# Optimization experiments

Measured on AMD Instinct MI355X. Metric: run time of the kernel, lower is better.

Reference implementation:

```python
import jax, jax.numpy as jnp
import numpy as np

B, S, H, W, T, D = 256, 128, 14, 14, 12, 512


def _lin(key, fan_in, fan_out):
    k1, k2 = jax.random.split(key)
    bound = 1.0 / np.sqrt(fan_in)
    Wm = jax.random.uniform(k1, (fan_in, fan_out), jnp.float32, -bound, bound)
    b = jax.random.uniform(k2, (fan_out,), jnp.float32, -bound, bound)
    return Wm, b


def setup_inputs() -> dict:
    key = jax.random.key(0)
    ks = jax.random.split(key, 20)
    inp = {
        "ci_1": jax.random.normal(ks[0], (B, D), jnp.float32),
        "mi_1": jax.random.normal(ks[1], (B, D), jnp.float32),
        "q": jax.random.normal(ks[2], (B, D), jnp.float32),
        "cws": jax.random.normal(ks[3], (B, S, D), jnp.float32),
        "K": jax.random.normal(ks[4], (B, H, W, D), jnp.float32),
        "C_past": jax.random.normal(ks[5], (B, T, D), jnp.float32),
        "M_past": jax.random.normal(ks[6], (B, T, D), jnp.float32),
    }
    inp["W_cq"], inp["b_cq"] = _lin(ks[7], D, D)          # control_qi
    inp["W_cqi"], inp["b_cqi"] = _lin(ks[8], 2 * D, D)    # cqi_linear
    inp["W_cai"], inp["b_cai"] = _lin(ks[9], D, 1)        # cais_linear
    inp["W_rm"], inp["b_rm"] = _lin(ks[10], D, D)         # memory_read_m
    inp["W_rk"], inp["b_rk"] = _lin(ks[11], D, D)         # memory_read_k
    inp["W_rik"], inp["b_rik"] = _lin(ks[12], 2 * D, D)   # memory_read_ik
    inp["W_rci"], inp["b_rci"] = _lin(ks[13], D, D)       # memory_read_ci_i
    inp["W_wrm"], inp["b_wrm"] = _lin(ks[14], 2 * D, D)   # memory_write_ri_mi_1
    inp["W_wcc"], inp["b_wcc"] = _lin(ks[15], D, 1)       # memory_write_ci_cj
    inp["W_wsa"], inp["b_wsa"] = _lin(ks[16], D, D)       # memory_write_mi_sa
    inp["W_winfo"], inp["b_winfo"] = _lin(ks[17], D, D)   # memory_write_mi_info
    inp["W_wci"], inp["b_wci"] = _lin(ks[18], D, 1)       # memory_write_ci
    return inp


def reference(ci_1, mi_1, q, cws, K, C_past, M_past,
              W_cq, b_cq, W_cqi, b_cqi, W_cai, b_cai,
              W_rm, b_rm, W_rk, b_rk, W_rik, b_rik, W_rci, b_rci,
              W_wrm, b_wrm, W_wcc, b_wcc, W_wsa, b_wsa,
              W_winfo, b_winfo, W_wci, b_wci):
    # ---- control ----
    qi = q @ W_cq + b_cq                                        # [B,D]
    cqi = jnp.concatenate([ci_1, qi], axis=1) @ W_cqi + b_cqi   # [B,D]
    cqi_cws = cqi[:, None, :] * cws                             # [B,S,D]
    cai = cqi_cws @ W_cai + b_cai                               # [B,S,1]
    cvis = jax.nn.softmax(cai, axis=1)
    ci = (cvis * cws).sum(axis=1)                               # [B,D]

    # ---- read ----
    Ii = (mi_1 @ W_rm + b_rm)[:, None, None, :] * (K @ W_rk + b_rk)  # [B,H,W,D]
    Ii_prime = jnp.concatenate([Ii, K], axis=3) @ W_rik + b_rik      # [B,H,W,D]
    rai = (ci[:, None, None, :] * Ii_prime) @ W_rci + b_rci          # [B,H,W,D]
    rvi = jax.nn.softmax(rai, axis=1)   # softmax over H
    rvi = jax.nn.softmax(rvi, axis=2)   # then softmax of those probs over W (faithful)
    ri = (rvi * K).sum(axis=(1, 2))                                  # [B,D]

    # ---- write ----
    mi_info = jnp.concatenate([ri, mi_1], axis=1) @ W_wrm + b_wrm    # [B,D]
    ci_cj = ci[:, None, :] * C_past                                  # [B,T,D]
    saij = jax.nn.softmax(ci_cj @ W_wcc + b_wcc, axis=1)             # [B,T,1]
    mi_sa = (saij * M_past).sum(axis=1)                              # [B,D]
    mi_prime = (mi_sa @ W_wsa + b_wsa) + (mi_info @ W_winfo + b_winfo)
    gate = jax.nn.sigmoid(ci @ W_wci + b_wci)                        # [B,1]
    mi = gate * mi_1 + (1.0 - gate) * mi_prime
    return (ci, mi)
```

## Files before the change

kernel.cpp:

```cpp
#include <hip/hip_runtime.h>
#include <hip/hip_bf16.h>

typedef unsigned short u16;
typedef __attribute__((ext_vector_type(8))) short short8;
typedef __attribute__((ext_vector_type(4))) float f4;

static __device__ __forceinline__ float b2f(u16 u) {
    union { unsigned int i; float f; } x; x.i = ((unsigned int)u) << 16; return x.f;
}
static __device__ __forceinline__ u16 f2b(float f) {
    union { float f; unsigned int i; } x; x.f = f;
    unsigned int r = x.i + 0x7fffu + ((x.i >> 16) & 1u);
    return (u16)(r >> 16);
}
static __device__ __forceinline__ float wave_reduce_sum(float v) {
    #pragma unroll
    for (int off = 32; off > 0; off >>= 1) v += __shfl_down(v, off, 64);
    return v;
}
static __device__ __forceinline__ void gl2lds(const void* g, void* l) {
    __builtin_amdgcn_global_load_lds(
        (const __attribute__((address_space(1))) void*)g,
        (__attribute__((address_space(3))) void*)l, 16, 0, 0);
}

__global__ __launch_bounds__(256) void conv_f32_bf16(
    const float* __restrict__ src, u16* __restrict__ dst, int n)
{
    int i = (blockIdx.x * 256 + threadIdx.x) * 4;
    if (i >= n) return;
    float4 v = *(const float4*)(src + i);
    union { u16 u[4]; uint2 d; } o;
    o.u[0] = f2b(v.x); o.u[1] = f2b(v.y); o.u[2] = f2b(v.z); o.u[3] = f2b(v.w);
    *(uint2*)(dst + i) = o.d;
}

__global__ __launch_bounds__(256) void transpose_k(
    const float* __restrict__ in, u16* __restrict__ out,
    int K, int N, int out_stride, int k_off)
{
    __shared__ float t[32][33];
    int kb = blockIdx.x * 32, nb = blockIdx.y * 32;
    int tx = threadIdx.x, ty = threadIdx.y;
    #pragma unroll
    for (int i = 0; i < 4; i++)
        t[ty + i * 8][tx] = in[(size_t)(kb + ty + i * 8) * N + nb + tx];
    __syncthreads();
    #pragma unroll
    for (int i = 0; i < 4; i++)
        out[(size_t)(nb + ty + i * 8) * out_stride + k_off + kb + tx] =
            f2b(t[tx][ty + i * 8]);
}

template<int MT, int NT>
__global__ __launch_bounds__(256) void gemm_mfma(
    const u16* __restrict__ A0, const u16* __restrict__ A1,
    int M, int K0, int K1, int N,
    const u16* __restrict__ Bt,
    const float* __restrict__ bias0, const float* __restrict__ bias1,
    int epi_mode, const float* __restrict__ E, int m_div,
    const float* __restrict__ gate, const float* __restrict__ mi1,
    void* __restrict__ Cout, int out_f32)
{
    constexpr int BM = MT * 32, BN = NT * 32;
    constexpr int STG = (BM + BN) * 32;
    constexpr int NPF = MT / 2 + NT / 2;
    constexpr int STAGE_B = 3 * STG * 2;
    constexpr int EP_B = (MT == 4) ? 32 * 260 * 4 : 0;
    __shared__ __align__(16) char smem[(STAGE_B > EP_B) ? STAGE_B : EP_B];
    short* stg = (short*)smem;
    float* ep  = (float*)smem;

    int tid  = threadIdx.x;
    int wave = tid >> 6, lane = tid & 63;
    int wm = wave >> 1, wn = wave & 1;
    int lrow = lane & 15, quad = lane >> 4;

    int gx = gridDim.x, gy = gridDim.y;
    int bx = blockIdx.x, by = blockIdx.y;
    if ((gy & 7) == 0) {
        int lin = by * gx + bx;
        int xcd = lin & 7, j = lin >> 3;
        by = xcd * (gy >> 3) + j / gx;
        bx = j % gx;
    }
    int bm0 = by * BM, bn0 = bx * BN;
    int Ktot = K0 + K1;
    int KT = Ktot >> 5;

    int r16 = lane >> 2, cc = lane & 3;
    int sw = (r16 >> 1) & 3;
    int coff = (cc ^ sw) * 8;

    auto stage = [&](int s, int k0) {
        const u16* asrc; int lda;
        if (k0 < K0) { asrc = A0 + k0; lda = K0; }
        else         { asrc = A1 + (k0 - K0); lda = K1; }
        short* As = stg + s * STG;
        short* Bs = As + BM * 32;
        #pragma unroll
        for (int i = 0; i < MT / 2; i++) {
            int ar = wave * (BM / 4) + 16 * i;
            gl2lds(asrc + (size_t)(bm0 + ar + r16) * lda + coff, As + ar * 32);
        }
        #pragma unroll
        for (int i = 0; i < NT / 2; i++) {
            int br = wave * (BN / 4) + 16 * i;
            gl2lds(Bt + (size_t)(bn0 + br + r16) * Ktot + k0 + coff, Bs + br * 32);
        }
    };

    f4 acc[MT][NT];
    #pragma unroll
    for (int i = 0; i < MT; i++)
        #pragma unroll
        for (int j = 0; j < NT; j++)
            acc[i][j] = (f4){0.f, 0.f, 0.f, 0.f};

    stage(0, 0);
    if (KT > 1) stage(1, 32);
    int sb = 0;
    int sw2 = (lrow >> 1) & 3;
    for (int kt = 0; kt < KT; kt++) {
        if (kt + 1 < KT) {
            if constexpr (NPF == 6)
                asm volatile("s_waitcnt vmcnt(6) lgkmcnt(0)\ns_barrier" ::: "memory");
            else if constexpr (NPF == 4)
                asm volatile("s_waitcnt vmcnt(4) lgkmcnt(0)\ns_barrier" ::: "memory");
            else if constexpr (NPF == 2)
                asm volatile("s_waitcnt vmcnt(2) lgkmcnt(0)\ns_barrier" ::: "memory");
            else
                asm volatile("s_waitcnt vmcnt(0) lgkmcnt(0)\ns_barrier" ::: "memory");
        } else {
            asm volatile("s_waitcnt vmcnt(0) lgkmcnt(0)\ns_barrier" ::: "memory");
        }
        const short* Ab = stg + sb * STG;
        const short* Bb = Ab + BM * 32;
        if (kt + 2 < KT) {
            int s2 = sb + 2; if (s2 >= 3) s2 -= 3;
            stage(s2, (kt + 2) * 32);
        }
        short8 af[MT], bfr[NT];
        #pragma unroll
        for (int mt = 0; mt < MT; mt++)
            af[mt] = *(const short8*)&Ab[(wm * (MT * 16) + mt * 16 + lrow) * 32 + (quad ^ sw2) * 8];
        #pragma unroll
        for (int nt = 0; nt < NT; nt++)
            bfr[nt] = *(const short8*)&Bb[(wn * (NT * 16) + nt * 16 + lrow) * 32 + (quad ^ sw2) * 8];
        #pragma unroll
        for (int mt = 0; mt < MT; mt++)
            #pragma unroll
            for (int nt = 0; nt < NT; nt++)
                acc[mt][nt] = __builtin_amdgcn_mfma_f32_16x16x32_bf16(
                    af[mt], bfr[nt], acc[mt][nt], 0, 0, 0);
        sb = (sb + 1 == 3) ? 0 : sb + 1;
    }

    if constexpr (MT == 4) {
        __syncthreads();
        int rr = tid >> 3, c8 = tid & 7;
        #pragma unroll
        for (int p = 0; p < 4; p++) {
            if (wm == (p >> 1)) {
                #pragma unroll
                for (int mh = 0; mh < 2; mh++) {
                    int mt = 2 * (p & 1) + mh;
                    int lm = mh * 16 + quad * 4;
                    #pragma unroll
                    for (int nt = 0; nt < NT; nt++) {
                        int col = wn * (NT * 16) + nt * 16 + lrow;
                        #pragma unroll
                        for (int r = 0; r < 4; r++)
                            ep[(lm + r) * 260 + col] = acc[mt][nt][r];
                    }
                }
            }
            __syncthreads();
            int m = bm0 + p * 32 + rr;
            #pragma unroll
            for (int i = 0; i < NT; i++) {
                int ci = i * 8 + c8;
                int n = bn0 + ci * 4;
                float4 v = *(const float4*)&ep[rr * 260 + ci * 4];
                if (bias0) {
                    float4 bb = *(const float4*)&bias0[n];
                    v.x += bb.x; v.y += bb.y; v.z += bb.z; v.w += bb.w;
                }
                if (bias1) {
                    float4 bb = *(const float4*)&bias1[n];
                    v.x += bb.x; v.y += bb.y; v.z += bb.z; v.w += bb.w;
                }
                if (epi_mode == 1) {
                    float4 e = *(const float4*)(E + (size_t)(m / m_div) * N + n);
                    v.x *= e.x; v.y *= e.y; v.z *= e.z; v.w *= e.w;
                } else if (epi_mode == 2) {
                    float g = gate[m];
                    float4 mm = *(const float4*)(mi1 + (size_t)m * N + n);
                    v.x = g * mm.x + (1.f - g) * v.x;
                    v.y = g * mm.y + (1.f - g) * v.y;
                    v.z = g * mm.z + (1.f - g) * v.z;
                    v.w = g * mm.w + (1.f - g) * v.w;
                }
                if (out_f32) {
                    *(float4*)((float*)Cout + (size_t)m * N + n) = v;
                } else {
                    union { u16 u[4]; uint2 d; } o;
                    o.u[0] = f2b(v.x); o.u[1] = f2b(v.y);
                    o.u[2] = f2b(v.z); o.u[3] = f2b(v.w);
                    *(uint2*)((u16*)Cout + (size_t)m * N + n) = o.d;
                }
            }
            __syncthreads();
        }
    } else {
        #pragma unroll
        for (int nt = 0; nt < NT; nt++) {
            int n = bn0 + wn * (NT * 16) + nt * 16 + lrow;
            float bv = 0.f;
            if (bias0) bv += bias0[n];
            if (bias1) bv += bias1[n];
            #pragma unroll
            for (int mt = 0; mt < MT; mt++) {
                #pragma unroll
                for (int r = 0; r < 4; r++) {
                    int m = bm0 + wm * (MT * 16) + mt * 16 + quad * 4 + r;
                    float v = acc[mt][nt][r] + bv;
                    if (epi_mode == 1) {
                        v *= E[(size_t)(m / m_div) * N + n];
                    } else if (epi_mode == 2) {
                        float g = gate[m];
                        v = g * mi1[(size_t)m * N + n] + (1.f - g) * v;
                    }
                    if (out_f32) ((float*)Cout)[(size_t)m * N + n] = v;
                    else         ((u16*)Cout)[(size_t)m * N + n] = f2b(v);
                }
            }
        }
    }
}

__global__ __launch_bounds__(256) void control_attn(
    const float* __restrict__ cqi, const float* __restrict__ cws,
    const float* __restrict__ Wcai, const float* __restrict__ bcai,
    float* __restrict__ ci_f32, float* __restrict__ ci_out)
{
    int b = blockIdx.x, tid = threadIdx.x;
    __shared__ float tW[512];
    __shared__ float p[128];
    __shared__ float inv_l;
    for (int d = tid; d < 512; d += 256)
        tW[d] = cqi[(size_t)b * 512 + d] * Wcai[d];
    __syncthreads();
    int wave = tid >> 6, lane = tid & 63;
    const float* cwsb = cws + (size_t)b * 128 * 512;
    for (int s = wave; s < 128; s += 4) {
        const float* row = cwsb + (size_t)s * 512 + lane * 8;
        float acc = 0.f;
        #pragma unroll
        for (int j = 0; j < 8; j++) acc += tW[lane * 8 + j] * row[j];
        acc = wave_reduce_sum(acc);
        if (lane == 0) p[s] = acc + bcai[0];
    }
    __syncthreads();
    if (tid == 0) {
        float m = -1e30f;
        for (int s = 0; s < 128; s++) m = fmaxf(m, p[s]);
        float l = 0.f;
        for (int s = 0; s < 128; s++) { float e = __expf(p[s] - m); p[s] = e; l += e; }
        inv_l = 1.f / l;
    }
    __syncthreads();
    float inv = inv_l;
    for (int d = tid; d < 512; d += 256) {
        float acc = 0.f;
        for (int s = 0; s < 128; s++) acc += p[s] * cwsb[(size_t)s * 512 + d];
        acc *= inv;
        ci_f32[(size_t)b * 512 + d] = acc;
        ci_out[(size_t)b * 512 + d] = acc;
    }
}

__global__ __launch_bounds__(256) void read_reduce(
    const u16* __restrict__ rai, const u16* __restrict__ Kb, u16* __restrict__ ri)
{
    int b = blockIdx.x >> 1;
    int d = ((blockIdx.x & 1) << 8) + threadIdx.x;
    const u16* rb = rai + (size_t)b * 196 * 512 + d;
    const u16* kb = Kb + (size_t)b * 196 * 512 + d;
    float m1[14], il1[14];
    #pragma unroll
    for (int w = 0; w < 14; w++) {
        float m = -1e30f, s = 0.f;
        #pragma unroll
        for (int h = 0; h < 14; h++) {
            float v = b2f(rb[(size_t)(h * 14 + w) * 512]);
            float nm = fmaxf(m, v);
            s = s * __expf(m - nm) + __expf(v - nm);
            m = nm;
        }
        m1[w] = m; il1[w] = 1.f / s;
    }
    float acc = 0.f;
    #pragma unroll
    for (int h = 0; h < 14; h++) {
        float pv[14], ss = 0.f;
        #pragma unroll
        for (int w = 0; w < 14; w++) {
            float pr = __expf(b2f(rb[(size_t)(h * 14 + w) * 512]) - m1[w]) * il1[w];
            float e = __expf(pr);
            pv[w] = e; ss += e;
        }
        float il2 = 1.f / ss;
        #pragma unroll
        for (int w = 0; w < 14; w++)
            acc += pv[w] * il2 * b2f(kb[(size_t)(h * 14 + w) * 512]);
    }
    ri[(size_t)b * 512 + d] = f2b(acc);
}

__global__ __launch_bounds__(256) void write_attn(
    const float* __restrict__ ci_f32, const float* __restrict__ C_past,
    const float* __restrict__ M_past,
    const float* __restrict__ Wwcc, const float* __restrict__ bwcc,
    const float* __restrict__ Wwci, const float* __restrict__ bwci,
    u16* __restrict__ mi_sa, float* __restrict__ gate)
{
    int b = blockIdx.x, tid = threadIdx.x;
    __shared__ float c[512];
    __shared__ float pt[12];
    __shared__ float red[256];
    for (int d = tid; d < 512; d += 256) c[d] = ci_f32[(size_t)b * 512 + d];
    __syncthreads();
    float g = 0.f;
    for (int d = tid; d < 512; d += 256) g += c[d] * Wwci[d];
    red[tid] = g;
    __syncthreads();
    for (int s = 128; s > 0; s >>= 1) {
        if (tid < s) red[tid] += red[tid + s];
        __syncthreads();
    }
    int wave = tid >> 6, lane = tid & 63;
    const float* cp = C_past + (size_t)b * 12 * 512;
    for (int t = wave; t < 12; t += 4) {
        float acc = 0.f;
        #pragma unroll
        for (int j = 0; j < 8; j++) {
            int d = lane * 8 + j;
            acc += c[d] * Wwcc[d] * cp[(size_t)t * 512 + d];
        }
        acc = wave_reduce_sum(acc);
        if (lane == 0) pt[t] = acc + bwcc[0];
    }
    __syncthreads();
    if (tid == 0) {
        float m = -1e30f;
        for (int t = 0; t < 12; t++) m = fmaxf(m, pt[t]);
        float l = 0.f;
        for (int t = 0; t < 12; t++) { float e = __expf(pt[t] - m); pt[t] = e; l += e; }
        float invl = 1.f / l;
        for (int t = 0; t < 12; t++) pt[t] *= invl;
        gate[b] = 1.f / (1.f + __expf(-(red[0] + bwci[0])));
    }
    __syncthreads();
    const float* mp = M_past + (size_t)b * 12 * 512;
    for (int d = tid; d < 512; d += 256) {
        float acc = 0.f;
        #pragma unroll
        for (int t = 0; t < 12; t++) acc += pt[t] * mp[(size_t)t * 512 + d];
        mi_sa[(size_t)b * 512 + d] = f2b(acc);
    }
}

extern "C" void kernel_launch(void* const* d_in, const int* in_sizes, int n_in,
                              void* d_out, int out_size, void* d_ws, size_t ws_size,
                              hipStream_t stream) {
    (void)in_sizes; (void)n_in; (void)out_size;
    const int B = 256, D = 512, HW = 196;

    const float* ci_1   = (const float*)d_in[0];
    const float* mi_1   = (const float*)d_in[1];
    const float* q      = (const float*)d_in[2];
    const float* cws    = (const float*)d_in[3];
    const float* Kin    = (const float*)d_in[4];
    const float* C_past = (const float*)d_in[5];
    const float* M_past = (const float*)d_in[6];
    const float* W_cq   = (const float*)d_in[7];
    const float* b_cq   = (const float*)d_in[8];
    const float* W_cqi  = (const float*)d_in[9];
    const float* b_cqi  = (const float*)d_in[10];
    const float* W_cai  = (const float*)d_in[11];
    const float* b_cai  = (const float*)d_in[12];
    const float* W_rm   = (const float*)d_in[13];
    const float* b_rm   = (const float*)d_in[14];
    const float* W_rk   = (const float*)d_in[15];
    const float* b_rk   = (const float*)d_in[16];
    const float* W_rik  = (const float*)d_in[17];
    const float* b_rik  = (const float*)d_in[18];
    const float* W_rci  = (const float*)d_in[19];
    const float* b_rci  = (const float*)d_in[20];
    const float* W_wrm  = (const float*)d_in[21];
    const float* b_wrm  = (const float*)d_in[22];
    const float* W_wcc  = (const float*)d_in[23];
    const float* b_wcc  = (const float*)d_in[24];
    const float* W_wsa  = (const float*)d_in[25];
    const float* b_wsa  = (const float*)d_in[26];
    const float* W_winfo= (const float*)d_in[27];
    const float* b_winfo= (const float*)d_in[28];
    const float* W_wci  = (const float*)d_in[29];
    const float* b_wci  = (const float*)d_in[30];

    float* out_ci = (float*)d_out;
    float* out_mi = (float*)d_out + (size_t)B * D;

    char* ws = (char*)d_ws;
    size_t off = 0;
    auto alloc = [&](size_t bytes) -> void* {
        void* p = ws + off; off += (bytes + 255) & ~(size_t)255; return p;
    };
    u16* wt_cq    = (u16*)alloc((size_t)D * D * 2);
    u16* wt_cqi   = (u16*)alloc((size_t)D * 2 * D * 2);
    u16* wt_rm    = (u16*)alloc((size_t)D * D * 2);
    u16* wt_rk    = (u16*)alloc((size_t)D * D * 2);
    u16* wt_rik   = (u16*)alloc((size_t)D * 2 * D * 2);
    u16* wt_rci   = (u16*)alloc((size_t)D * D * 2);
    u16* wt_wrm   = (u16*)alloc((size_t)D * 2 * D * 2);
    u16* wt_wsi   = (u16*)alloc((size_t)D * 2 * D * 2);
    u16* qb       = (u16*)alloc((size_t)B * D * 2);
    u16* cib      = (u16*)alloc((size_t)B * D * 2);
    u16* mib      = (u16*)alloc((size_t)B * D * 2);
    u16* qi_buf   = (u16*)alloc((size_t)B * D * 2);
    float* cqi_f32= (float*)alloc((size_t)B * D * 4);
    float* rm_f32 = (float*)alloc((size_t)B * D * 4);
    float* ci_f32 = (float*)alloc((size_t)B * D * 4);
    u16* ri_buf   = (u16*)alloc((size_t)B * D * 2);
    u16* misa_buf = (u16*)alloc((size_t)B * D * 2);
    u16* minfo_buf= (u16*)alloc((size_t)B * D * 2);
    float* gate_b = (float*)alloc((size_t)B * 4);

    int chunk_b = 256;
    while (chunk_b > 32) {
        size_t need = off + 3 * (((size_t)chunk_b * HW * D * 2 + 255) & ~(size_t)255);
        if (need <= ws_size) break;
        chunk_b >>= 1;
    }
    u16* kbf  = (u16*)alloc((size_t)chunk_b * HW * D * 2);
    u16* big1 = (u16*)alloc((size_t)chunk_b * HW * D * 2);
    u16* big2 = (u16*)alloc((size_t)chunk_b * HW * D * 2);

    dim3 tb(32, 8);
    transpose_k<<<dim3(D / 32, D / 32), tb, 0, stream>>>(W_cq,   wt_cq,  D,     D, D,     0);
    transpose_k<<<dim3(2 * D / 32, D / 32), tb, 0, stream>>>(W_cqi, wt_cqi, 2 * D, D, 2 * D, 0);
    transpose_k<<<dim3(D / 32, D / 32), tb, 0, stream>>>(W_rm,   wt_rm,  D,     D, D,     0);
    transpose_k<<<dim3(D / 32, D / 32), tb, 0, stream>>>(W_rk,   wt_rk,  D,     D, D,     0);
    transpose_k<<<dim3(2 * D / 32, D / 32), tb, 0, stream>>>(W_rik, wt_rik, 2 * D, D, 2 * D, 0);
    transpose_k<<<dim3(D / 32, D / 32), tb, 0, stream>>>(W_rci,  wt_rci, D,     D, D,     0);
    transpose_k<<<dim3(2 * D / 32, D / 32), tb, 0, stream>>>(W_wrm, wt_wrm, 2 * D, D, 2 * D, 0);
    transpose_k<<<dim3(D / 32, D / 32), tb, 0, stream>>>(W_wsa,  wt_wsi, D,     D, 2 * D, 0);
    transpose_k<<<dim3(D / 32, D / 32), tb, 0, stream>>>(W_winfo,wt_wsi, D,     D, 2 * D, D);

    int nbd = B * D;
    conv_f32_bf16<<<nbd / 1024, 256, 0, stream>>>(q, qb, nbd);
    conv_f32_bf16<<<nbd / 1024, 256, 0, stream>>>(ci_1, cib, nbd);
    conv_f32_bf16<<<nbd / 1024, 256, 0, stream>>>(mi_1, mib, nbd);

    dim3 gsmall(D / 64, B / 64);

    gemm_mfma<2,2><<<gsmall, 256, 0, stream>>>(qb, nullptr, B, D, 0, D, wt_cq, b_cq, nullptr,
                                               0, nullptr, 1, nullptr, nullptr, qi_buf, 0);
    gemm_mfma<2,2><<<gsmall, 256, 0, stream>>>(cib, qi_buf, B, D, D, D, wt_cqi, b_cqi, nullptr,
                                               0, nullptr, 1, nullptr, nullptr, cqi_f32, 1);
    control_attn<<<B, 256, 0, stream>>>(cqi_f32, cws, W_cai, b_cai, ci_f32, out_ci);
    gemm_mfma<2,2><<<gsmall, 256, 0, stream>>>(mib, nullptr, B, D, 0, D, wt_rm, b_rm, nullptr,
                                               0, nullptr, 1, nullptr, nullptr, rm_f32, 1);

    for (int c = 0; c < B; c += chunk_b) {
        int mrows = chunk_b * HW;
        const float* Kc = Kin + (size_t)c * HW * D;
        conv_f32_bf16<<<(mrows * D) / 1024, 256, 0, stream>>>(Kc, kbf, mrows * D);
        dim3 gbig(D / 128, mrows / 128);
        gemm_mfma<4,4><<<gbig, 256, 0, stream>>>(kbf, nullptr, mrows, D, 0, D, wt_rk, b_rk, nullptr,
                                                 1, rm_f32 + (size_t)c * D, HW, nullptr, nullptr,
                                                 big1, 0);
        gemm_mfma<4,4><<<gbig, 256, 0, stream>>>(big1, kbf, mrows, D, D, D, wt_rik, b_rik, nullptr,
                                                 1, ci_f32 + (size_t)c * D, HW, nullptr, nullptr,
                                                 big2, 0);
        gemm_mfma<4,4><<<gbig, 256, 0, stream>>>(big2, nullptr, mrows, D, 0, D, wt_rci, b_rci, nullptr,
                                                 0, nullptr, 1, nullptr, nullptr, big1, 0);
        read_reduce<<<chunk_b * 2, 256, 0, stream>>>(big1, kbf, ri_buf + (size_t)c * D);
    }

    gemm_mfma<2,2><<<gsmall, 256, 0, stream>>>(ri_buf, mib, B, D, D, D, wt_wrm, b_wrm, nullptr,
                                               0, nullptr, 1, nullptr, nullptr, minfo_buf, 0);
    write_attn<<<B, 256, 0, stream>>>(ci_f32, C_past, M_past, W_wcc, b_wcc, W_wci, b_wci,
                                      misa_buf, gate_b);
    gemm_mfma<2,2><<<gsmall, 256, 0, stream>>>(misa_buf, minfo_buf, B, D, D, D, wt_wsi,
                                               b_wsa, b_winfo, 2, nullptr, 1, gate_b, mi_1,
                                               out_mi, 1);
}
```

Baseline: 597.8 us.

## Fuse the three read-stage GEMMs into one kernel keeping intermediates in LDS

Result: slower. 634.6 us (+6.2%).

```diff
diff --git a/kernel.cpp b/kernel.cpp
--- a/kernel.cpp
+++ b/kernel.cpp
@@ -66,10 +66,8 @@
     constexpr int STG = (BM + BN) * 32;
     constexpr int NPF = MT / 2 + NT / 2;
     constexpr int STAGE_B = 3 * STG * 2;
-    constexpr int EP_B = (MT == 4) ? 32 * 260 * 4 : 0;
-    __shared__ __align__(16) char smem[(STAGE_B > EP_B) ? STAGE_B : EP_B];
+    __shared__ __align__(16) char smem[STAGE_B];
     short* stg = (short*)smem;
-    float* ep  = (float*)smem;
 
     int tid  = threadIdx.x;
     int wave = tid >> 6, lane = tid & 63;
@@ -123,11 +121,7 @@
     int sw2 = (lrow >> 1) & 3;
     for (int kt = 0; kt < KT; kt++) {
         if (kt + 1 < KT) {
-            if constexpr (NPF == 6)
-                asm volatile("s_waitcnt vmcnt(6) lgkmcnt(0)\ns_barrier" ::: "memory");
-            else if constexpr (NPF == 4)
-                asm volatile("s_waitcnt vmcnt(4) lgkmcnt(0)\ns_barrier" ::: "memory");
-            else if constexpr (NPF == 2)
+            if constexpr (NPF == 2)
                 asm volatile("s_waitcnt vmcnt(2) lgkmcnt(0)\ns_barrier" ::: "memory");
             else
                 asm volatile("s_waitcnt vmcnt(0) lgkmcnt(0)\ns_barrier" ::: "memory");
@@ -156,86 +150,201 @@
         sb = (sb + 1 == 3) ? 0 : sb + 1;
     }
 
-    if constexpr (MT == 4) {
-        __syncthreads();
-        int rr = tid >> 3, c8 = tid & 7;
-        #pragma unroll
-        for (int p = 0; p < 4; p++) {
-            if (wm == (p >> 1)) {
-                #pragma unroll
-                for (int mh = 0; mh < 2; mh++) {
-                    int mt = 2 * (p & 1) + mh;
-                    int lm = mh * 16 + quad * 4;
-                    #pragma unroll
-                    for (int nt = 0; nt < NT; nt++) {
-                        int col = wn * (NT * 16) + nt * 16 + lrow;
-                        #pragma unroll
-                        for (int r = 0; r < 4; r++)
-                            ep[(lm + r) * 260 + col] = acc[mt][nt][r];
-                    }
-                }
-            }
-            __syncthreads();
-            int m = bm0 + p * 32 + rr;
+    #pragma unroll
+    for (int nt = 0; nt < NT; nt++) {
+        int n = bn0 + wn * (NT * 16) + nt * 16 + lrow;
+        float bv = 0.f;
+        if (bias0) bv += bias0[n];
+        if (bias1) bv += bias1[n];
+        #pragma unroll
+        for (int mt = 0; mt < MT; mt++) {
             #pragma unroll
-            for (int i = 0; i < NT; i++) {
-                int ci = i * 8 + c8;
-                int n = bn0 + ci * 4;
-                float4 v = *(const float4*)&ep[rr * 260 + ci * 4];
-                if (bias0) {
-                    float4 bb = *(const float4*)&bias0[n];
-                    v.x += bb.x; v.y += bb.y; v.z += bb.z; v.w += bb.w;
-                }
-                if (bias1) {
-                    float4 bb = *(const float4*)&bias1[n];
-                    v.x += bb.x; v.y += bb.y; v.z += bb.z; v.w += bb.w;
-                }
+            for (int r = 0; r < 4; r++) {
+                int m = bm0 + wm * (MT * 16) + mt * 16 + quad * 4 + r;
+                float v = acc[mt][nt][r] + bv;
                 if (epi_mode == 1) {
-                    float4 e = *(const float4*)(E + (size_t)(m / m_div) * N + n);
-                    v.x *= e.x; v.y *= e.y; v.z *= e.z; v.w *= e.w;
+                    v *= E[(size_t)(m / m_div) * N + n];
                 } else if (epi_mode == 2) {
                     float g = gate[m];
-                    float4 mm = *(const float4*)(mi1 + (size_t)m * N + n);
-                    v.x = g * mm.x + (1.f - g) * v.x;
-                    v.y = g * mm.y + (1.f - g) * v.y;
-                    v.z = g * mm.z + (1.f - g) * v.z;
-                    v.w = g * mm.w + (1.f - g) * v.w;
+                    v = g * mi1[(size_t)m * N + n] + (1.f - g) * v;
                 }
-                if (out_f32) {
-                    *(float4*)((float*)Cout + (size_t)m * N + n) = v;
-                } else {
-                    union { u16 u[4]; uint2 d; } o;
-                    o.u[0] = f2b(v.x); o.u[1] = f2b(v.y);
-                    o.u[2] = f2b(v.z); o.u[3] = f2b(v.w);
-                    *(uint2*)((u16*)Cout + (size_t)m * N + n) = o.d;
-                }
+                if (out_f32) ((float*)Cout)[(size_t)m * N + n] = v;
+                else         ((u16*)Cout)[(size_t)m * N + n] = f2b(v);
             }
-            __syncthreads();
-        }
-    } else {
-        #pragma unroll
-        for (int nt = 0; nt < NT; nt++) {
-            int n = bn0 + wn * (NT * 16) + nt * 16 + lrow;
-            float bv = 0.f;
-            if (bias0) bv += bias0[n];
-            if (bias1) bv += bias1[n];
+        }
+    }
+}
+
+__global__ __launch_bounds__(512, 2) void fused_read(
+    const u16* __restrict__ kbf, int M,
+    const u16* __restrict__ Wrk,  const float* __restrict__ brk,  const float* __restrict__ E1,
+    const u16* __restrict__ Wrik, const float* __restrict__ brik, const float* __restrict__ E2,
+    const u16* __restrict__ Wrci, const float* __restrict__ brci,
+    u16* __restrict__ rai)
+{
+    __shared__ __align__(16) char smem[139264];
+    short* g_tile = (short*)smem;
+    short* stgbase = (short*)(smem + 65536);
+
+    int tid = threadIdx.x, wave = tid >> 6, lane = tid & 63;
+    int wr = wave >> 2, wc = wave & 3;
+    int lrow = lane & 15, quad = lane >> 4;
+    int r16 = lane >> 2, cc = lane & 3;
+    int sw = (r16 >> 1) & 3;
+    int coff = (cc ^ sw) * 8;
+    int sw2 = (lrow >> 1) & 3;
+
+    int bid = blockIdx.x;
+    { int nb = gridDim.x; if ((nb & 7) == 0) { int x = bid & 7, j = bid >> 3; bid = x * (nb >> 3) + j; } }
+    int bm0 = bid * 64;
+
+    auto stageB = [&](short* bf, const u16* Wt, int ldk, int k0) {
+        short* Bs = bf + 2048;
+        #pragma unroll
+        for (int i = 0; i < 4; i++) {
+            int br = wave * 64 + i * 16;
+            gl2lds(Wt + (size_t)(br + r16) * ldk + k0 + coff, Bs + br * 32);
+        }
+    };
+    auto stageA = [&](short* bf, int k0) {
+        if (wave < 4) {
+            int ar = wave * 16;
+            gl2lds(kbf + (size_t)(bm0 + ar + r16) * 512 + k0 + coff, bf + ar * 32);
+        }
+    };
+
+    f4 acc[2][8];
+    auto clr = [&]() {
+        #pragma unroll
+        for (int t = 0; t < 2; t++)
             #pragma unroll
-            for (int mt = 0; mt < MT; mt++) {
+            for (int nt = 0; nt < 8; nt++)
+                acc[t][nt] = (f4){0.f, 0.f, 0.f, 0.f};
+    };
+
+    auto kstep = [&](const short* bf, int aMode, int kc0) {
+        short8 af[2], bfrag[8];
+        #pragma unroll
+        for (int t = 0; t < 2; t++) {
+            int R = wr * 32 + t * 16 + lrow;
+            if (aMode == 0)
+                af[t] = *(const short8*)&bf[R * 32 + (quad ^ sw2) * 8];
+            else {
+                int kc = kc0 + quad;
+                af[t] = *(const short8*)&g_tile[R * 512 + ((kc ^ (R & 7)) << 3)];
+            }
+        }
+        const short* Bs = bf + 2048;
+        #pragma unroll
+        for (int nt = 0; nt < 8; nt++)
+            bfrag[nt] = *(const short8*)&Bs[(wc * 128 + nt * 16 + lrow) * 32 + (quad ^ sw2) * 8];
+        #pragma unroll
+        for (int t = 0; t < 2; t++)
+            #pragma unroll
+            for (int nt = 0; nt < 8; nt++)
+                acc[t][nt] = __builtin_amdgcn_mfma_f32_16x16x32_bf16(
+                    af[t], bfrag[nt], acc[t][nt], 0, 0, 0);
+    };
+
+    int b0 = bm0 / 196, b1 = (bm0 + 63) / 196;
+    int rsw = (b1 != b0) ? (b1 * 196 - bm0) : 64;
+    auto epi_to_gtile = [&](const float* bias, const float* E) {
+        #pragma unroll
+        for (int nt = 0; nt < 8; nt++) {
+            int n = wc * 128 + nt * 16 + lrow;
+            float bv = bias[n];
+            float e0 = E[(size_t)b0 * 512 + n];
+            float e1 = E[(size_t)b1 * 512 + n];
+            #pragma unroll
+            for (int t = 0; t < 2; t++)
                 #pragma unroll
                 for (int r = 0; r < 4; r++) {
-                    int m = bm0 + wm * (MT * 16) + mt * 16 + quad * 4 + r;
-                    float v = acc[mt][nt][r] + bv;
-                    if (epi_mode == 1) {
-                        v *= E[(size_t)(m / m_div) * N + n];
-                    } else if (epi_mode == 2) {
-                        float g = gate[m];
-                        v = g * mi1[(size_t)m * N + n] + (1.f - g) * v;
-                    }
-                    if (out_f32) ((float*)Cout)[(size_t)m * N + n] = v;
-                    else         ((u16*)Cout)[(size_t)m * N + n] = f2b(v);
+                    int row = wr * 32 + t * 16 + quad * 4 + r;
+                    float e = (row < rsw) ? e0 : e1;
+                    u16 h = f2b((acc[t][nt][r] + bv) * e);
+                    int chunk = (n >> 3) ^ (row & 7);
+                    g_tile[row * 512 + chunk * 8 + (n & 7)] = (short)h;
                 }
+        }
+    };
+
+    clr();
+    stageA(stgbase, 0); stageB(stgbase, Wrk, 512, 0);
+    for (int kt = 0; kt < 16; kt++) {
+        short* cur = stgbase + (kt & 1) * 18432;
+        short* nxt = stgbase + ((kt & 1) ^ 1) * 18432;
+        if (kt + 1 < 16) {
+            stageA(nxt, (kt + 1) * 32); stageB(nxt, Wrk, 512, (kt + 1) * 32);
+            if (wave < 4) asm volatile("s_waitcnt vmcnt(5) lgkmcnt(0)\ns_barrier" ::: "memory");
+            else          asm volatile("s_waitcnt vmcnt(4) lgkmcnt(0)\ns_barrier" ::: "memory");
+        } else
+            asm volatile("s_waitcnt vmcnt(0) lgkmcnt(0)\ns_barrier" ::: "memory");
+        kstep(cur, 0, 0);
+        __syncthreads();
+    }
+    epi_to_gtile(brk, E1);
+    __syncthreads();
+
+    clr();
+    stageB(stgbase, Wrik, 1024, 0);
+    for (int kt = 0; kt < 16; kt++) {
+        short* cur = stgbase + (kt & 1) * 18432;
+        short* nxt = stgbase + ((kt & 1) ^ 1) * 18432;
+        if (kt + 1 < 16) {
+            stageB(nxt, Wrik, 1024, (kt + 1) * 32);
+            asm volatile("s_waitcnt vmcnt(4) lgkmcnt(0)\ns_barrier" ::: "memory");
+        } else
+            asm volatile("s_waitcnt vmcnt(0) lgkmcnt(0)\ns_barrier" ::: "memory");
+        kstep(cur, 1, kt * 4);
+        __syncthreads();
+    }
+    stageA(stgbase, 0); stageB(stgbase, Wrik, 1024, 512);
+    for (int kt = 0; kt < 16; kt++) {
+        short* cur = stgbase + (kt & 1) * 18432;
+        short* nxt = stgbase + ((kt & 1) ^ 1) * 18432;
+        if (kt + 1 < 16) {
+            stageA(nxt, (kt + 1) * 32); stageB(nxt, Wrik, 1024, 512 + (kt + 1) * 32);
+            if (wave < 4) asm volatile("s_waitcnt vmcnt(5) lgkmcnt(0)\ns_barrier" ::: "memory");
+            else          asm volatile("s_waitcnt vmcnt(4) lgkmcnt(0)\ns_barrier" ::: "memory");
+        } else
+            asm volatile("s_waitcnt vmcnt(0) lgkmcnt(0)\ns_barrier" ::: "memory");
+        kstep(cur, 0, 0);
+        __syncthreads();
+    }
+    epi_to_gtile(brik, E2);
+    __syncthreads();
+
+    clr();
+    stageB(stgbase, Wrci, 512, 0);
+    for (int kt = 0; kt < 16; kt++) {
+        short* cur = stgbase + (kt & 1) * 18432;
+        short* nxt = stgbase + ((kt & 1) ^ 1) * 18432;
+        if (kt + 1 < 16) {
+            stageB(nxt, Wrci, 512, (kt + 1) * 32);
+            asm volatile("s_waitcnt vmcnt(4) lgkmcnt(0)\ns_barrier" ::: "memory");
+        } else
+            asm volatile("s_waitcnt vmcnt(0) lgkmcnt(0)\ns_barrier" ::: "memory");
+        kstep(cur, 1, kt * 4);
+        __syncthreads();
+    }
+    #pragma unroll
+    for (int nt = 0; nt < 8; nt++) {
+        int n = wc * 128 + nt * 16 + lrow;
+        float bv = brci[n];
+        #pragma unroll
+        for (int t = 0; t < 2; t++)
+            #pragma unroll
+            for (int r = 0; r < 4; r++) {
+                int row = wr * 32 + t * 16 + quad * 4 + r;
+                g_tile[row * 512 + n] = (short)f2b(acc[t][nt][r] + bv);
             }
-        }
+    }
+    __syncthreads();
+    #pragma unroll
+    for (int p = 0; p < 8; p++) {
+        int idx = p * 512 + tid;
+        short8 v = *(const short8*)&g_tile[idx * 8];
+        *(short8*)&rai[(size_t)bm0 * 512 + (size_t)idx * 8] = v;
     }
 }
 
@@ -439,13 +548,12 @@
 
     int chunk_b = 256;
     while (chunk_b > 32) {
-        size_t need = off + 3 * (((size_t)chunk_b * HW * D * 2 + 255) & ~(size_t)255);
+        size_t need = off + 2 * (((size_t)chunk_b * HW * D * 2 + 255) & ~(size_t)255);
         if (need <= ws_size) break;
         chunk_b >>= 1;
     }
     u16* kbf  = (u16*)alloc((size_t)chunk_b * HW * D * 2);
     u16* big1 = (u16*)alloc((size_t)chunk_b * HW * D * 2);
-    u16* big2 = (u16*)alloc((size_t)chunk_b * HW * D * 2);
 
     dim3 tb(32, 8);
     transpose_k<<<dim3(D / 32, D / 32), tb, 0, stream>>>(W_cq,   wt_cq,  D,     D, D,     0);
@@ -477,15 +585,12 @@
         int mrows = chunk_b * HW;
         const float* Kc = Kin + (size_t)c * HW * D;
         conv_f32_bf16<<<(mrows * D) / 1024, 256, 0, stream>>>(Kc, kbf, mrows * D);
-        dim3 gbig(D / 128, mrows / 128);
-        gemm_mfma<4,4><<<gbig, 256, 0, stream>>>(kbf, nullptr, mrows, D, 0, D, wt_rk, b_rk, nullptr,
-                                                 1, rm_f32 + (size_t)c * D, HW, nullptr, nullptr,
-                                                 big1, 0);
-        gemm_mfma<4,4><<<gbig, 256, 0, stream>>>(big1, kbf, mrows, D, D, D, wt_rik, b_rik, nullptr,
-                                                 1, ci_f32 + (size_t)c * D, HW, nullptr, nullptr,
-                                                 big2, 0);
-        gemm_mfma<4,4><<<gbig, 256, 0, stream>>>(big2, nullptr, mrows, D, 0, D, wt_rci, b_rci, nullptr,
-                                                 0, nullptr, 1, nullptr, nullptr, big1, 0);
+        fused_read<<<mrows / 64, 512, 0, stream>>>(
+            kbf, mrows,
+            wt_rk,  b_rk,  rm_f32 + (size_t)c * D,
+            wt_rik, b_rik, ci_f32 + (size_t)c * D,
+            wt_rci, b_rci,
+            big1);
         read_reduce<<<chunk_b * 2, 256, 0, stream>>>(big1, kbf, ri_buf + (size_t)c * D);
     }
 
```
